# Kernel optimization log

Hardware: AMD Instinct MI355X
Metric: run time of the kernel (lower is better)

Reference implementation:

```python
import jax, jax.numpy as jnp
import numpy as np

B, P, ENC = 64, 196, 2048
ATT, DEC, EMB = 512, 512, 512
V, MAXLEN = 10000, 30


def setup_inputs() -> dict:
    key = jax.random.key(0)
    ks = jax.random.split(key, 20)
    s = 0.02
    inp = {
        "encoder_out": jax.random.normal(ks[0], (B, P, ENC), jnp.float32),
        "captions": jax.random.randint(ks[1], (B, MAXLEN), 0, V).astype(jnp.int64),
        "caption_lengths": jax.random.randint(ks[2], (B,), 1, MAXLEN).astype(jnp.int64),
        # parameters (PyTorch Linear convention: y = x @ W.T + b)
        "emb_table": jax.random.uniform(ks[3], (V, EMB), jnp.float32, -0.1, 0.1),
        "W_enc_att": jax.random.normal(ks[4], (ATT, ENC), jnp.float32) * s,
        "b_enc_att": jnp.zeros((ATT,), jnp.float32),
        "W_dec_att": jax.random.normal(ks[5], (ATT, DEC), jnp.float32) * s,
        "b_dec_att": jnp.zeros((ATT,), jnp.float32),
        "w_full_att": jax.random.normal(ks[6], (1, ATT), jnp.float32) * s,
        "b_full_att": jnp.zeros((1,), jnp.float32),
        "W_ih": jax.random.normal(ks[7], (4 * DEC, EMB + ENC), jnp.float32) * s,
        "b_ih": jnp.zeros((4 * DEC,), jnp.float32),
        "W_hh": jax.random.normal(ks[8], (4 * DEC, DEC), jnp.float32) * s,
        "b_hh": jnp.zeros((4 * DEC,), jnp.float32),
        "W_init_h": jax.random.normal(ks[9], (DEC, ENC), jnp.float32) * s,
        "b_init_h": jnp.zeros((DEC,), jnp.float32),
        "W_init_c": jax.random.normal(ks[10], (DEC, ENC), jnp.float32) * s,
        "b_init_c": jnp.zeros((DEC,), jnp.float32),
        "W_fc": jax.random.uniform(ks[11], (V, DEC), jnp.float32, -0.1, 0.1),
        "b_fc": jnp.zeros((V,), jnp.float32),
    }
    return inp


def reference(encoder_out, captions, caption_lengths, emb_table,
              W_enc_att, b_enc_att, W_dec_att, b_dec_att,
              w_full_att, b_full_att, W_ih, b_ih, W_hh, b_hh,
              W_init_h, b_init_h, W_init_c, b_init_c, W_fc, b_fc):
    # init hidden state from mean-pooled encoder features
    mean_enc = encoder_out.mean(axis=1)                       # [B, ENC]
    h0 = mean_enc @ W_init_h.T + b_init_h                     # [B, DEC]
    c0 = mean_enc @ W_init_c.T + b_init_c                     # [B, DEC]

    # encoder-side attention projection is time-invariant: hoist out of the loop
    att1 = jnp.einsum('bpe,ae->bpa', encoder_out, W_enc_att) + b_enc_att  # [B, P, ATT]

    embeddings = emb_table[captions]                          # [B, T, EMB]
    T = captions.shape[1] - 1
    emb_steps = jnp.swapaxes(embeddings[:, :T, :], 0, 1)      # [T, B, EMB]

    def step(carry, emb_t):
        h, c = carry
        att2 = h @ W_dec_att.T + b_dec_att                    # [B, ATT]
        e = (jax.nn.relu(att1 + att2[:, None, :]) @ w_full_att.T + b_full_att)[..., 0]  # [B, P]
        alpha = jax.nn.softmax(e, axis=1)                     # [B, P]
        context = jnp.einsum('bp,bpe->be', alpha, encoder_out)  # [B, ENC]
        x = jnp.concatenate([emb_t, context], axis=1)         # [B, EMB+ENC]
        gates = x @ W_ih.T + b_ih + h @ W_hh.T + b_hh         # [B, 4*DEC]
        i, f, g, o = jnp.split(gates, 4, axis=1)
        c_new = jax.nn.sigmoid(f) * c + jax.nn.sigmoid(i) * jnp.tanh(g)
        h_new = jax.nn.sigmoid(o) * jnp.tanh(c_new)
        preds = h_new @ W_fc.T + b_fc                         # dropout in eval mode = identity
        return (h_new, c_new), (preds, alpha)

    _, (preds_seq, alpha_seq) = jax.lax.scan(step, (h0, c0), emb_steps)
    predictions = jnp.swapaxes(preds_seq, 0, 1)               # [B, T, V]
    alphas = jnp.swapaxes(alpha_seq, 0, 1)                    # [B, T, P]
    return predictions, alphas
```

## Files before the change

kernel.cpp:

```cpp
#include <hip/hip_runtime.h>
#include <cstddef>

constexpr int B_   = 64;
constexpr int P_   = 196;
constexpr int ENC_ = 2048;
constexpr int ATT_ = 512;
constexpr int DEC_ = 512;
constexpr int EMB_ = 512;
constexpr int V_   = 10000;
constexpr int MAXLEN_ = 30;
constexpr int T_   = 29;
constexpr int G4_  = 2048;
constexpr int KIH_ = 2560;
constexpr int XK2_ = 2560;

constexpr int NBLK = 256;
constexpr int TPB  = 1024;
constexpr int NT   = NBLK * TPB;
constexpr int NW   = NT / 64;
constexpr int FSTR = 16;
constexpr size_t ZS_ = (size_t)B_ * G4_;
constexpr int NPT = 625;

typedef __attribute__((ext_vector_type(8))) short short8;
typedef __attribute__((ext_vector_type(4))) float f32x4;
using us = unsigned short;

__device__ __forceinline__ us f2bf(float x) {
    union { float f; unsigned u; } v; v.f = x;
    unsigned r = v.u + 0x7fff + ((v.u >> 16) & 1);
    return (us)(r >> 16);
}
__device__ __forceinline__ float bf2f(us u) {
    union { unsigned u; float f; } v; v.u = ((unsigned)u) << 16;
    return v.f;
}

__device__ __forceinline__ unsigned ld4cc(const void* p) {
    unsigned r;
    asm volatile("global_load_dword %0, %1, off sc1\n\ts_waitcnt vmcnt(0)"
                 : "=v"(r) : "v"(p) : "memory");
    return r;
}
__device__ __forceinline__ void ld4cc_x8(const float* p0, const float* p1,
                                         const float* p2, const float* p3,
                                         const float* p4, const float* p5,
                                         const float* p6, const float* p7,
                                         float* o) {
    float r0, r1, r2, r3, r4, r5, r6, r7;
    asm volatile("global_load_dword %0, %8, off sc1\n\t"
                 "global_load_dword %1, %9, off sc1\n\t"
                 "global_load_dword %2, %10, off sc1\n\t"
                 "global_load_dword %3, %11, off sc1\n\t"
                 "global_load_dword %4, %12, off sc1\n\t"
                 "global_load_dword %5, %13, off sc1\n\t"
                 "global_load_dword %6, %14, off sc1\n\t"
                 "global_load_dword %7, %15, off sc1\n\t"
                 "s_waitcnt vmcnt(0)"
                 : "=&v"(r0), "=&v"(r1), "=&v"(r2), "=&v"(r3),
                   "=&v"(r4), "=&v"(r5), "=&v"(r6), "=&v"(r7)
                 : "v"(p0), "v"(p1), "v"(p2), "v"(p3),
                   "v"(p4), "v"(p5), "v"(p6), "v"(p7) : "memory");
    o[0]=r0; o[1]=r1; o[2]=r2; o[3]=r3; o[4]=r4; o[5]=r5; o[6]=r6; o[7]=r7;
}
__device__ __forceinline__ void ld16cc_x3(const void* p0, const void* p1, const void* p2,
                                          short8* a, short8* b, short8* c) {
    short8 ra, rb, rc;
    asm volatile("global_load_dwordx4 %0, %3, off sc1\n\t"
                 "global_load_dwordx4 %1, %4, off sc1\n\t"
                 "global_load_dwordx4 %2, %5, off sc1\n\t"
                 "s_waitcnt vmcnt(0)"
                 : "=&v"(ra), "=&v"(rb), "=&v"(rc)
                 : "v"(p0), "v"(p1), "v"(p2) : "memory");
    *a = ra; *b = rb; *c = rc;
}
__device__ __forceinline__ void ld16cc_x4(const void* p0, const void* p1,
                                          const void* p2, const void* p3,
                                          short8* a, short8* b, short8* c, short8* d) {
    short8 ra, rb, rc, rd;
    asm volatile("global_load_dwordx4 %0, %4, off sc1\n\t"
                 "global_load_dwordx4 %1, %5, off sc1\n\t"
                 "global_load_dwordx4 %2, %6, off sc1\n\t"
                 "global_load_dwordx4 %3, %7, off sc1\n\t"
                 "s_waitcnt vmcnt(0)"
                 : "=&v"(ra), "=&v"(rb), "=&v"(rc), "=&v"(rd)
                 : "v"(p0), "v"(p1), "v"(p2), "v"(p3) : "memory");
    *a = ra; *b = rb; *c = rc; *d = rd;
}
__device__ __forceinline__ void ldf8cc(const void* p0, const void* p1, f32x4* a, f32x4* b) {
    f32x4 ra, rb;
    asm volatile("global_load_dwordx4 %0, %2, off sc1\n\t"
                 "global_load_dwordx4 %1, %3, off sc1\n\t"
                 "s_waitcnt vmcnt(0)"
                 : "=&v"(ra), "=&v"(rb) : "v"(p0), "v"(p1) : "memory");
    *a = ra; *b = rb;
}
__device__ __forceinline__ void st4cc(void* p, unsigned v) {
    asm volatile("global_store_dword %0, %1, off sc1" :: "v"(p), "v"(v) : "memory");
}
__device__ __forceinline__ void st2cc(void* p, unsigned v) {
    asm volatile("global_store_short %0, %1, off sc1" :: "v"(p), "v"(v) : "memory");
}
__device__ __forceinline__ float wredsum(float a) {
#pragma unroll
    for (int o = 32; o > 0; o >>= 1) a += __shfl_xor(a, o);
    return a;
}

template<bool REL>
__device__ __forceinline__ void gbar_arrive(unsigned* flags, unsigned tok) {
    asm volatile("s_waitcnt vmcnt(0)" ::: "memory");
    __syncthreads();
    if (threadIdx.x == 0)
        __hip_atomic_store(&flags[blockIdx.x * FSTR], tok,
                           REL ? __ATOMIC_RELEASE : __ATOMIC_RELAXED,
                           __HIP_MEMORY_SCOPE_AGENT);
}
__device__ __forceinline__ void gbar_wait(unsigned* flags, unsigned tok) {
    if (threadIdx.x < NBLK) {
        while (__hip_atomic_load(&flags[threadIdx.x * FSTR], __ATOMIC_RELAXED,
                                 __HIP_MEMORY_SCOPE_AGENT) < tok)
            __builtin_amdgcn_s_sleep(1);
    }
    __syncthreads();
}
template<bool REL>
__device__ __forceinline__ void gbar(unsigned* flags, unsigned tok) {
    gbar_arrive<REL>(flags, tok);
    gbar_wait(flags, tok);
}

__device__ __forceinline__ void cvt8(const float* __restrict__ src, us* __restrict__ dst) {
    const float4* p = (const float4*)src;
    float4 a = p[0], b = p[1];
    union { short8 v; us u[8]; } o;
    o.u[0] = f2bf(a.x); o.u[1] = f2bf(a.y); o.u[2] = f2bf(a.z); o.u[3] = f2bf(a.w);
    o.u[4] = f2bf(b.x); o.u[5] = f2bf(b.y); o.u[6] = f2bf(b.z); o.u[7] = f2bf(b.w);
    *(short8*)dst = o.v;
}

__device__ __forceinline__ float score8(short8 v, const f32x4& lo, const f32x4& hi,
                                        const float4& w0, const float4& w1) {
    float acc = 0.f, x;
    x = bf2f((us)v[0]) + lo[0]; acc += fmaxf(x, 0.f) * w0.x;
    x = bf2f((us)v[1]) + lo[1]; acc += fmaxf(x, 0.f) * w0.y;
    x = bf2f((us)v[2]) + lo[2]; acc += fmaxf(x, 0.f) * w0.z;
    x = bf2f((us)v[3]) + lo[3]; acc += fmaxf(x, 0.f) * w0.w;
    x = bf2f((us)v[4]) + hi[0]; acc += fmaxf(x, 0.f) * w1.x;
    x = bf2f((us)v[5]) + hi[1]; acc += fmaxf(x, 0.f) * w1.y;
    x = bf2f((us)v[6]) + hi[2]; acc += fmaxf(x, 0.f) * w1.z;
    x = bf2f((us)v[7]) + hi[3]; acc += fmaxf(x, 0.f) * w1.w;
    return acc;
}

__device__ __forceinline__ void preds_task(const us* s_h, const us* __restrict__ wfcb,
                                           const float* __restrict__ b_fc,
                                           float* __restrict__ outp,
                                           int nt, int tt, int lane) {
    const int r = lane & 15, g = lane >> 4;
    f32x4 acc[4] = {{0,0,0,0},{0,0,0,0},{0,0,0,0},{0,0,0,0}};
    const us* Brow = wfcb + (size_t)(nt*16 + r)*DEC_ + g*8;
    const us* As   = s_h + r*520 + g*8;
#pragma unroll
    for (int k0 = 0; k0 < DEC_; k0 += 64) {
        short8 b0 = *(const short8*)(Brow + k0);
        short8 b1 = *(const short8*)(Brow + k0 + 32);
#pragma unroll
        for (int mt = 0; mt < 4; ++mt) {
            short8 a0 = *(const short8*)(As + mt*16*520 + k0);
            short8 a1 = *(const short8*)(As + mt*16*520 + k0 + 32);
            acc[mt] = __builtin_amdgcn_mfma_f32_16x16x32_bf16(a0, b0, acc[mt], 0, 0, 0);
            acc[mt] = __builtin_amdgcn_mfma_f32_16x16x32_bf16(a1, b1, acc[mt], 0, 0, 0);
        }
    }
    const int n = nt*16 + r;
    const float bv = b_fc[n];
#pragma unroll
    for (int mt = 0; mt < 4; ++mt)
#pragma unroll
        for (int i = 0; i < 4; ++i) {
            int b = mt*16 + g*4 + i;
            outp[(size_t)b*(T_*V_) + (size_t)tt*V_ + n] = acc[mt][i] + bv;
        }
}

__global__ __launch_bounds__(TPB) void k_persist(
    const float* __restrict__ enc, const int* __restrict__ captions,
    const float* __restrict__ emb_table,
    const float* __restrict__ W_enc_att, const float* __restrict__ b_enc_att,
    const float* __restrict__ W_dec_att, const float* __restrict__ b_dec_att,
    const float* __restrict__ w_full,
    const float* __restrict__ W_ih, const float* __restrict__ b_ih,
    const float* __restrict__ W_hh, const float* __restrict__ b_hh,
    const float* __restrict__ W_init_h, const float* __restrict__ b_init_h,
    const float* __restrict__ W_init_c, const float* __restrict__ b_init_c,
    const float* __restrict__ W_fc, const float* __restrict__ b_fc,
    us* encb, us* wencb, us* wdecb, us* wfcb, us* wcat2, us* wembW,
    us* winitb, us* xembA, us* att1b, us* hbuf, us* xcatb, us* meanbb,
    float* cst, float* att2G, float* gp, float* gpe, float* bsum,
    unsigned* flags, float* outp, float* outa)
{
    __shared__ us s_stage[64 * 520];
    __shared__ us s_wb[64 * 328];
    __shared__ us s_wd[16 * 520];
    __shared__ float s_e[P_];
    __shared__ float s_al[P_];
    __shared__ float s_red[32];

    const int tid = threadIdx.x, bid = blockIdx.x;
    const int gtid = bid * TPB + tid;
    const int wid  = gtid >> 6;
    const int w    = tid >> 6;
    const int lane = tid & 63;
    unsigned tok = 0;
    float creg = 0.f;
    us* const hb0 = hbuf;
    us* const hb1 = hbuf + (size_t)B_ * DEC_;

    for (int i = gtid; i < B_*P_*ENC_/8; i += NT) cvt8(enc + (size_t)i*8, encb + (size_t)i*8);
    for (int i = gtid; i < ATT_*ENC_/8; i += NT) cvt8(W_enc_att + (size_t)i*8, wencb + (size_t)i*8);
    for (int i = gtid; i < ATT_*DEC_/8; i += NT) cvt8(W_dec_att + (size_t)i*8, wdecb + (size_t)i*8);
    for (int i = gtid; i < V_*DEC_/8;   i += NT) cvt8(W_fc + (size_t)i*8, wfcb + (size_t)i*8);
    for (int i = gtid; i < G4_*XK2_/8;  i += NT) {
        int n = (i*8) / XK2_, k = (i*8) % XK2_;
        const float* src = (k < ENC_) ? (W_ih + (size_t)n*KIH_ + EMB_ + k)
                                      : (W_hh + (size_t)n*DEC_ + (k - ENC_));
        cvt8(src, wcat2 + (size_t)i*8);
    }
    for (int i = gtid; i < G4_*EMB_/8;  i += NT)
        cvt8(W_ih + ((size_t)((i*8) / EMB_))*KIH_ + ((i*8) % EMB_), wembW + (size_t)i*8);
    for (int i = gtid; i < 1024*ENC_/8; i += NT) {
        int n = (i*8) >> 11, k = (i*8) & (ENC_ - 1);
        const float* src = (n < 512) ? (W_init_h + (size_t)n*ENC_ + k)
                                     : (W_init_c + (size_t)(n-512)*ENC_ + k);
        cvt8(src, winitb + (size_t)i*8);
    }
    for (int i = gtid; i < T_*B_*EMB_/8; i += NT) {
        int r = i >> 6, c8 = i & 63;
        int t = r >> 6, b = r & 63;
        int cap = captions[b*MAXLEN_ + t];
        cvt8(emb_table + (size_t)cap*EMB_ + c8*8, xembA + (size_t)r*EMB_ + c8*8);
    }
    if (gtid < G4_) bsum[gtid] = b_ih[gtid] + b_hh[gtid];
    if (gtid < B_*ENC_) {
        int b = gtid >> 11, e = gtid & (ENC_ - 1);
        const float* base = enc + (size_t)b*P_*ENC_ + e;
        float s = 0.f;
        for (int p = 0; p < P_; ++p) s += base[(size_t)p*ENC_];
        meanbb[gtid] = f2bf(s * (1.f / P_));
    }
    gbar<true>(flags, ++tok);

    for (int task = wid; task < 256 + 1856; task += NW) {
        const int r = lane & 15, g = lane >> 4;
        if (task < 256) {
            const int mt = task & 3, nt = task >> 2;
            const int m0 = mt*16, n0 = nt*16;
            const us* Ar = meanbb + (size_t)(m0 + r)*ENC_ + g*8;
            const us* Br = winitb + (size_t)(n0 + r)*ENC_ + g*8;
            f32x4 acc0 = {0,0,0,0}, acc1 = {0,0,0,0};
#pragma unroll 4
            for (int k0 = 0; k0 < ENC_; k0 += 64) {
                acc0 = __builtin_amdgcn_mfma_f32_16x16x32_bf16(
                    *(const short8*)(Ar + k0), *(const short8*)(Br + k0), acc0, 0, 0, 0);
                acc1 = __builtin_amdgcn_mfma_f32_16x16x32_bf16(
                    *(const short8*)(Ar + k0 + 32), *(const short8*)(Br + k0 + 32), acc1, 0, 0, 0);
            }
            const int n = n0 + r;
            if (n < 512) {
                float bv = b_init_h[n];
#pragma unroll
                for (int i = 0; i < 4; ++i) {
                    int b = m0 + g*4 + i;
                    unsigned hv = f2bf(acc0[i] + acc1[i] + bv);
                    st2cc(hb1 + b*DEC_ + n, hv);
                    st2cc(xcatb + (size_t)b*XK2_ + ENC_ + n, hv);
                }
            } else {
                int d = n - 512;
                float bv = b_init_c[d];
#pragma unroll
                for (int i = 0; i < 4; ++i)
                    st4cc(cst + (m0 + g*4 + i)*DEC_ + d,
                          __float_as_uint(acc0[i] + acc1[i] + bv));
            }
        } else {
            const int q = task - 256;
            const int m0 = (q >> 6) * 64, n0 = (q & 63) * 32;
            f32x4 acc[4][2] = {};
            const us* Ab = xembA + (size_t)(m0 + r)*EMB_ + g*8;
            const us* Bb = wembW + (size_t)(n0 + r)*EMB_ + g*8;
#pragma unroll 2
            for (int k0 = 0; k0 < EMB_; k0 += 32) {
                short8 af[4], bfr[2];
#pragma unroll
                for (int mi = 0; mi < 4; ++mi)
                    af[mi] = *(const short8*)(Ab + (size_t)mi*16*EMB_ + k0);
#pragma unroll
                for (int nj = 0; nj < 2; ++nj)
                    bfr[nj] = *(const short8*)(Bb + (size_t)nj*16*EMB_ + k0);
#pragma unroll
                for (int mi = 0; mi < 4; ++mi)
#pragma unroll
                    for (int nj = 0; nj < 2; ++nj)
                        acc[mi][nj] = __builtin_amdgcn_mfma_f32_16x16x32_bf16(
                            af[mi], bfr[nj], acc[mi][nj], 0, 0, 0);
            }
#pragma unroll
            for (int mi = 0; mi < 4; ++mi)
#pragma unroll
                for (int nj = 0; nj < 2; ++nj) {
                    int n = n0 + nj*16 + r;
                    float bv = bsum[n];
#pragma unroll
                    for (int i = 0; i < 4; ++i) {
                        int m = m0 + mi*16 + g*4 + i;
                        gpe[(size_t)m*G4_ + n] = acc[mi][nj][i] + bv;
                    }
                }
        }
    }
    gbar<true>(flags, ++tok);

    for (int task = wid; task < 3264; task += NW) {
        const int r = lane & 15, g = lane >> 4;
        if (task < 3136) {
            int mt = task >> 4, nt2 = task & 15;
            int m0 = mt*64, n0 = nt2*32;
            f32x4 acc[4][2] = {};
            const us* Ab = encb + (size_t)(m0 + r)*ENC_ + g*8;
            const us* Bb = wencb + (size_t)(n0 + r)*ENC_ + g*8;
#pragma unroll 2
            for (int k0 = 0; k0 < ENC_; k0 += 32) {
                short8 af[4], bfr[2];
#pragma unroll
                for (int mi = 0; mi < 4; ++mi)
                    af[mi] = *(const short8*)(Ab + (size_t)mi*16*ENC_ + k0);
#pragma unroll
                for (int nj = 0; nj < 2; ++nj)
                    bfr[nj] = *(const short8*)(Bb + (size_t)nj*16*ENC_ + k0);
#pragma unroll
                for (int mi = 0; mi < 4; ++mi)
#pragma unroll
                    for (int nj = 0; nj < 2; ++nj)
                        acc[mi][nj] = __builtin_amdgcn_mfma_f32_16x16x32_bf16(
                            af[mi], bfr[nj], acc[mi][nj], 0, 0, 0);
            }
#pragma unroll
            for (int mi = 0; mi < 4; ++mi)
#pragma unroll
                for (int nj = 0; nj < 2; ++nj) {
                    int n = n0 + nj*16 + r;
                    float bv = b_enc_att[n];
#pragma unroll
                    for (int i = 0; i < 4; ++i) {
                        int m = m0 + mi*16 + g*4 + i;
                        att1b[(size_t)m*ATT_ + n] = f2bf(acc[mi][nj][i] + bv);
                    }
                }
        } else {
            int q = task - 3136;
            int nt = q >> 2, mt = q & 3;
            const us* Ar = hb1 + (size_t)(mt*16 + r)*DEC_ + g*8;
            const us* Br = wdecb + (size_t)(nt*16 + r)*DEC_ + g*8;
            f32x4 acc0 = {0,0,0,0}, acc1 = {0,0,0,0};
#pragma unroll 4
            for (int k0 = 0; k0 < DEC_; k0 += 64) {
                short8 a0, a1, dum;
                ld16cc_x3(Ar + k0, Ar + k0 + 32, Ar + k0, &a0, &a1, &dum);
                acc0 = __builtin_amdgcn_mfma_f32_16x16x32_bf16(
                    a0, *(const short8*)(Br + k0), acc0, 0, 0, 0);
                acc1 = __builtin_amdgcn_mfma_f32_16x16x32_bf16(
                    a1, *(const short8*)(Br + k0 + 32), acc1, 0, 0, 0);
            }
            int n = nt*16 + r;
            float bv = b_dec_att[n];
#pragma unroll
            for (int i = 0; i < 4; ++i)
                st4cc(att2G + (size_t)(mt*16 + g*4 + i)*ATT_ + n,
                      __float_as_uint(acc0[i] + acc1[i] + bv));
        }
    }
    gbar<true>(flags, ++tok);

    {
        const int z = bid >> 5, nb = bid & 31;
        for (int c = tid; c < 2560; c += TPB) {
            int row = c / 40, col8 = c % 40;
            *(short8*)(s_wb + row*328 + col8*8) =
                *(const short8*)(wcat2 + (size_t)(nb*64 + row)*XK2_ + (size_t)z*320 + col8*8);
        }
        if (bid < 32)
            for (int c = tid; c < 1024; c += TPB) {
                int row = c >> 6, col8 = c & 63;
                *(short8*)(s_wd + row*520 + col8*8) =
                    *(const short8*)(wdecb + (size_t)(bid*16 + row)*DEC_ + col8*8);
            }
        if (tid < 128) creg = __uint_as_float(ld4cc(cst + bid*128 + tid));
        __syncthreads();
    }

    for (int t = 0; t < T_; ++t) {
        {
            const int b = bid & 63, cc = bid >> 6;
            f32x4 a2lo, a2hi;
            const float* ap = att2G + (size_t)b*ATT_ + lane*8;
            ldf8cc(ap, ap + 4, &a2lo, &a2hi);
            const float4 w0 = *(const float4*)(w_full + lane*8);
            const float4 w1 = *(const float4*)(w_full + lane*8 + 4);
            const us* a1base = att1b + (size_t)b*P_*ATT_ + lane*8;
            for (int p = w; p < P_; p += 32) {
                const int p2 = p + 16;
                short8 v0 = *(const short8*)(a1base + (size_t)p*ATT_);
                short8 v1 = (p2 < P_) ? *(const short8*)(a1base + (size_t)p2*ATT_) : v0;
                float acc0 = score8(v0, a2lo, a2hi, w0, w1);
                float acc1 = score8(v1, a2lo, a2hi, w0, w1);
                acc0 = wredsum(acc0);
                acc1 = wredsum(acc1);
                if (lane == 0) {
                    s_e[p] = acc0;
                    if (p2 < P_) s_e[p2] = acc1;
                }
            }
            __syncthreads();
            float v = (tid < P_) ? s_e[tid] : -3.4e38f;
            float mx = v;
#pragma unroll
            for (int o = 32; o > 0; o >>= 1) mx = fmaxf(mx, __shfl_xor(mx, o));
            if (lane == 0) s_red[w] = mx;
            __syncthreads();
            mx = s_red[0];
#pragma unroll
            for (int j = 1; j < 16; ++j) mx = fmaxf(mx, s_red[j]);
            float ev = (tid < P_) ? expf(v - mx) : 0.f;
            float sm = wredsum(ev);
            if (lane == 0) s_red[16 + w] = sm;
            __syncthreads();
            float tot = 0.f;
#pragma unroll
            for (int j = 0; j < 16; ++j) tot += s_red[16 + j];
            if (tid < P_) {
                float al = ev / tot;
                s_al[tid] = al;
                if (cc == 0) outa[((size_t)b*T_ + t)*P_ + tid] = al;
            }
            __syncthreads();
            float a[8] = {};
            const us* ep = encb + (size_t)b*P_*ENC_ + cc*512 + lane*8;
            for (int p = w; p < P_; p += 16) {
                short8 vv = *(const short8*)(ep + (size_t)p*ENC_);
                float al = s_al[p];
#pragma unroll
                for (int j = 0; j < 8; ++j) a[j] += al * bf2f((us)vv[j]);
            }
            float* s_accf = (float*)s_stage;
            {
                f32x4 lo = {a[0],a[1],a[2],a[3]}, hi = {a[4],a[5],a[6],a[7]};
                *(f32x4*)(s_accf + w*512 + lane*8)     = lo;
                *(f32x4*)(s_accf + w*512 + lane*8 + 4) = hi;
            }
            __syncthreads();
            if (tid < 256) {
                int c2 = tid*2;
                float s0 = 0.f, s1 = 0.f;
#pragma unroll
                for (int q = 0; q < 16; ++q) {
                    s0 += s_accf[q*512 + c2];
                    s1 += s_accf[q*512 + c2 + 1];
                }
                unsigned pk = (unsigned)f2bf(s0) | ((unsigned)f2bf(s1) << 16);
                st4cc(xcatb + (size_t)b*XK2_ + cc*512 + c2, pk);
            }
            __syncthreads();
        }
        gbar<false>(flags, ++tok);

        {
            const int z = bid >> 5;
            {
                short8 v0, v1, v2;
                int c0 = tid, c1 = tid + 1024, c2i = tid + 2048;
                const us* p0 = xcatb + (size_t)(c0/40)*XK2_ + z*320 + (c0%40)*8;
                const us* p1 = xcatb + (size_t)(c1/40)*XK2_ + z*320 + (c1%40)*8;
                bool has2 = c2i < 2560;
                const us* p2 = has2 ? xcatb + (size_t)(c2i/40)*XK2_ + z*320 + (c2i%40)*8 : p0;
                ld16cc_x3(p0, p1, p2, &v0, &v1, &v2);
                *(short8*)(s_stage + (c0/40)*328 + (c0%40)*8) = v0;
                *(short8*)(s_stage + (c1/40)*328 + (c1%40)*8) = v1;
                if (has2) *(short8*)(s_stage + (c2i/40)*328 + (c2i%40)*8) = v2;
            }
            __syncthreads();
            const int nt = (bid & 31)*4 + (w >> 2), mt = w & 3;
            const int r = lane & 15, g = lane >> 4;
            const us* sxr = s_stage + (mt*16 + r)*328 + g*8;
            const us* Br  = s_wb + ((w >> 2)*16 + r)*328 + g*8;
            f32x4 acc0 = {0,0,0,0}, acc1 = {0,0,0,0};
#pragma unroll
            for (int k0 = 0; k0 < 320; k0 += 64) {
                acc0 = __builtin_amdgcn_mfma_f32_16x16x32_bf16(
                    *(const short8*)(sxr + k0), *(const short8*)(Br + k0), acc0, 0, 0, 0);
                acc1 = __builtin_amdgcn_mfma_f32_16x16x32_bf16(
                    *(const short8*)(sxr + k0 + 32), *(const short8*)(Br + k0 + 32), acc1, 0, 0, 0);
            }
            const int n = nt*16 + r;
#pragma unroll
            for (int i = 0; i < 4; ++i) {
                int m = mt*16 + g*4 + i;
                st4cc(gp + ZS_*z + (size_t)m*G4_ + n, __float_as_uint(acc0[i] + acc1[i]));
            }
            __syncthreads();
        }
        gbar<false>(flags, ++tok);

        {
            float* sg = (float*)s_stage;
            if (tid < 512) {
                const int cell = tid & 127, gate = tid >> 7;
                const int idx = bid*128 + cell;
                const int b = idx >> 9, d = idx & 511;
                const float* gz = gp + (size_t)b*G4_ + gate*512 + d;
                float vz[8];
                ld4cc_x8(gz, gz + ZS_, gz + 2*ZS_, gz + 3*ZS_,
                         gz + 4*ZS_, gz + 5*ZS_, gz + 6*ZS_, gz + 7*ZS_, vz);
                sg[tid] = ((vz[0]+vz[1]) + (vz[2]+vz[3])) + ((vz[4]+vz[5]) + (vz[6]+vz[7]));
            }
            __syncthreads();
            if (tid < 128) {
                const int idx = bid*128 + tid;
                const int b = idx >> 9, d = idx & 511;
                const float* ge = gpe + ((size_t)(t*B_ + b))*G4_ + d;
                float gi = sg[tid]       + ge[0];
                float gf = sg[128 + tid] + ge[512];
                float gg = sg[256 + tid] + ge[1024];
                float go = sg[384 + tid] + ge[1536];
                float si = 1.f / (1.f + expf(-gi));
                float sf = 1.f / (1.f + expf(-gf));
                float so = 1.f / (1.f + expf(-go));
                float cn = sf * creg + si * tanhf(gg);
                creg = cn;
                float hn = so * tanhf(cn);
                unsigned hv = f2bf(hn);
                us* hnew = (t & 1) ? hb1 : hb0;
                st2cc(hnew + idx, hv);
                st2cc(xcatb + (size_t)b*XK2_ + ENC_ + d, hv);
            }
        }
        gbar<false>(flags, ++tok);

        if (t != T_ - 1) {
            ++tok;
            if (bid < 32) {
                {
                    const us* hbn = (t & 1) ? hb1 : hb0;
                    short8 v0, v1, v2, v3;
                    int c0 = tid, c1 = tid + 1024, c2i = tid + 2048, c3 = tid + 3072;
                    ld16cc_x4(hbn + (c0>>6)*DEC_ + (c0&63)*8, hbn + (c1>>6)*DEC_ + (c1&63)*8,
                              hbn + (c2i>>6)*DEC_ + (c2i&63)*8, hbn + (c3>>6)*DEC_ + (c3&63)*8,
                              &v0, &v1, &v2, &v3);
                    *(short8*)(s_stage + (c0>>6)*520 + (c0&63)*8) = v0;
                    *(short8*)(s_stage + (c1>>6)*520 + (c1&63)*8) = v1;
                    *(short8*)(s_stage + (c2i>>6)*520 + (c2i&63)*8) = v2;
                    *(short8*)(s_stage + (c3>>6)*520 + (c3&63)*8) = v3;
                }
                __syncthreads();
                if (w < 4) {
                    const int r = lane & 15, g = lane >> 4;
                    const us* As = s_stage + (w*16 + r)*520 + g*8;
                    const us* Bs = s_wd + r*520 + g*8;
                    f32x4 acc0 = {0,0,0,0}, acc1 = {0,0,0,0};
#pragma unroll
                    for (int k0 = 0; k0 < DEC_; k0 += 64) {
                        acc0 = __builtin_amdgcn_mfma_f32_16x16x32_bf16(
                            *(const short8*)(As + k0), *(const short8*)(Bs + k0), acc0, 0, 0, 0);
                        acc1 = __builtin_amdgcn_mfma_f32_16x16x32_bf16(
                            *(const short8*)(As + k0 + 32), *(const short8*)(Bs + k0 + 32), acc1, 0, 0, 0);
                    }
                    const int n = bid*16 + r;
                    float bv = b_dec_att[n];
#pragma unroll
                    for (int i = 0; i < 4; ++i)
                        st4cc(att2G + (size_t)(w*16 + g*4 + i)*ATT_ + n,
                              __float_as_uint(acc0[i] + acc1[i] + bv));
                }
                gbar_arrive<false>(flags, tok);
                gbar_wait(flags, tok);
            } else {
                gbar_arrive<false>(flags, tok);
                if (t > 0) {
                    const us* hbo = (t & 1) ? hb0 : hb1;
                    short8 v0, v1, v2, v3;
                    int c0 = tid, c1 = tid + 1024, c2i = tid + 2048, c3 = tid + 3072;
                    ld16cc_x4(hbo + (c0>>6)*DEC_ + (c0&63)*8, hbo + (c1>>6)*DEC_ + (c1&63)*8,
                              hbo + (c2i>>6)*DEC_ + (c2i&63)*8, hbo + (c3>>6)*DEC_ + (c3&63)*8,
                              &v0, &v1, &v2, &v3);
                    *(short8*)(s_stage + (c0>>6)*520 + (c0&63)*8) = v0;
                    *(short8*)(s_stage + (c1>>6)*520 + (c1&63)*8) = v1;
                    *(short8*)(s_stage + (c2i>>6)*520 + (c2i&63)*8) = v2;
                    *(short8*)(s_stage + (c3>>6)*520 + (c3&63)*8) = v3;
                    __syncthreads();
                    const int tq = (bid - 32)*3 + w;
                    if (w < 3 && tq < NPT)
                        preds_task(s_stage, wfcb, b_fc, outp, tq, t - 1, lane);
                }
                gbar_wait(flags, tok);
            }
        } else {
            if (bid >= 32) {
                const us* hbo = (t & 1) ? hb0 : hb1;
                short8 v0, v1, v2, v3;
                int c0 = tid, c1 = tid + 1024, c2i = tid + 2048, c3 = tid + 3072;
                ld16cc_x4(hbo + (c0>>6)*DEC_ + (c0&63)*8, hbo + (c1>>6)*DEC_ + (c1&63)*8,
                          hbo + (c2i>>6)*DEC_ + (c2i&63)*8, hbo + (c3>>6)*DEC_ + (c3&63)*8,
                          &v0, &v1, &v2, &v3);
                *(short8*)(s_stage + (c0>>6)*520 + (c0&63)*8) = v0;
                *(short8*)(s_stage + (c1>>6)*520 + (c1&63)*8) = v1;
                *(short8*)(s_stage + (c2i>>6)*520 + (c2i&63)*8) = v2;
                *(short8*)(s_stage + (c3>>6)*520 + (c3&63)*8) = v3;
                __syncthreads();
                const int tq = (bid - 32)*3 + w;
                if (w < 3 && tq < NPT)
                    preds_task(s_stage, wfcb, b_fc, outp, tq, t - 1, lane);
            }
        }
    }

    if (bid < 40) {
        __syncthreads();
        const us* hbn = ((T_ - 1) & 1) ? hb1 : hb0;
        {
            short8 v0, v1, v2, v3;
            int c0 = tid, c1 = tid + 1024, c2i = tid + 2048, c3 = tid + 3072;
            ld16cc_x4(hbn + (c0>>6)*DEC_ + (c0&63)*8, hbn + (c1>>6)*DEC_ + (c1&63)*8,
                      hbn + (c2i>>6)*DEC_ + (c2i&63)*8, hbn + (c3>>6)*DEC_ + (c3&63)*8,
                      &v0, &v1, &v2, &v3);
            *(short8*)(s_stage + (c0>>6)*520 + (c0&63)*8) = v0;
            *(short8*)(s_stage + (c1>>6)*520 + (c1&63)*8) = v1;
            *(short8*)(s_stage + (c2i>>6)*520 + (c2i&63)*8) = v2;
            *(short8*)(s_stage + (c3>>6)*520 + (c3&63)*8) = v3;
        }
        __syncthreads();
        const int tq = bid*16 + w;
        if (tq < NPT)
            preds_task(s_stage, wfcb, b_fc, outp, tq, T_ - 1, lane);
    }
}

extern "C" void kernel_launch(void* const* d_in, const int* in_sizes, int n_in,
                              void* d_out, int out_size, void* d_ws, size_t ws_size,
                              hipStream_t stream) {
    const float* enc       = (const float*)d_in[0];
    const int*   captions  = (const int*)d_in[1];
    const float* emb_table = (const float*)d_in[3];
    const float* W_enc_att = (const float*)d_in[4];
    const float* b_enc_att = (const float*)d_in[5];
    const float* W_dec_att = (const float*)d_in[6];
    const float* b_dec_att = (const float*)d_in[7];
    const float* w_full    = (const float*)d_in[8];
    const float* W_ih      = (const float*)d_in[10];
    const float* b_ih      = (const float*)d_in[11];
    const float* W_hh      = (const float*)d_in[12];
    const float* b_hh      = (const float*)d_in[13];
    const float* W_init_h  = (const float*)d_in[14];
    const float* b_init_h  = (const float*)d_in[15];
    const float* W_init_c  = (const float*)d_in[16];
    const float* b_init_c  = (const float*)d_in[17];
    const float* W_fc      = (const float*)d_in[18];
    const float* b_fc      = (const float*)d_in[19];

    char* ws = (char*)d_ws;
    size_t off = 0;
    auto alloc = [&](size_t bytes) {
        void* p = ws + off;
        off = (off + bytes + 255) & ~(size_t)255;
        return p;
    };
    us* encb   = (us*)alloc((size_t)B_ * P_ * ENC_ * 2);
    us* wencb  = (us*)alloc((size_t)ATT_ * ENC_ * 2);
    us* wdecb  = (us*)alloc((size_t)ATT_ * DEC_ * 2);
    us* wfcb   = (us*)alloc((size_t)V_ * DEC_ * 2);
    us* wcat2  = (us*)alloc((size_t)G4_ * XK2_ * 2);
    us* wembW  = (us*)alloc((size_t)G4_ * EMB_ * 2);
    us* winitb = (us*)alloc((size_t)1024 * ENC_ * 2);
    us* xembA  = (us*)alloc((size_t)T_ * B_ * EMB_ * 2);
    us* att1b  = (us*)alloc((size_t)B_ * P_ * ATT_ * 2);
    us* hbuf   = (us*)alloc((size_t)2 * B_ * DEC_ * 2);
    us* xcatb  = (us*)alloc((size_t)B_ * XK2_ * 2);
    us* meanbb = (us*)alloc((size_t)B_ * ENC_ * 2);
    float* cst   = (float*)alloc((size_t)B_ * DEC_ * 4);
    float* att2G = (float*)alloc((size_t)B_ * ATT_ * 4);
    float* gp    = (float*)alloc((size_t)B_ * G4_ * 8 * 4);
    float* gpe   = (float*)alloc((size_t)T_ * B_ * G4_ * 4);
    float* bsum  = (float*)alloc((size_t)G4_ * 4);
    unsigned* flags = (unsigned*)alloc((size_t)(NBLK + 1) * FSTR * 4);

    float* outp = (float*)d_out;
    float* outa = outp + (size_t)B_ * T_ * V_;

    hipMemsetAsync(flags, 0, (NBLK + 1) * FSTR * sizeof(unsigned), stream);
    k_persist<<<NBLK, TPB, 0, stream>>>(
        enc, captions, emb_table, W_enc_att, b_enc_att, W_dec_att, b_dec_att,
        w_full, W_ih, b_ih, W_hh, b_hh, W_init_h, b_init_h, W_init_c, b_init_c,
        W_fc, b_fc,
        encb, wencb, wdecb, wfcb, wcat2, wembW, winitb, xembA, att1b, hbuf, xcatb,
        meanbb, cst, att2G, gp, gpe, bsum, flags, outp, outa);
}
```

Before: 1.204 ms.

## Fuse att2 projection into LSTM cell blocks as split-K partials, drop a grid barrier

Each block that produces a slice of the new hidden state now computes a partial att2 product (a 128-wide K chunk of W_dec_att) right away and writes it to a partial-sum buffer. The attention stage later sums the four partials when it loads att2. This removes the separate att2 MFMA phase on 32 blocks and one grid-wide barrier per timestep, and spreads the fc prediction work across all blocks. The trade-off is scalar FMA work reading W_dec_att from global memory in every block, four times the att2 loads, and some added per-block latency before the barrier.

```diff
diff --git a/kernel.cpp b/kernel.cpp
--- a/kernel.cpp
+++ b/kernel.cpp
@@ -87,13 +87,24 @@
                  : "v"(p0), "v"(p1), "v"(p2), "v"(p3) : "memory");
     *a = ra; *b = rb; *c = rc; *d = rd;
 }
-__device__ __forceinline__ void ldf8cc(const void* p0, const void* p1, f32x4* a, f32x4* b) {
-    f32x4 ra, rb;
-    asm volatile("global_load_dwordx4 %0, %2, off sc1\n\t"
-                 "global_load_dwordx4 %1, %3, off sc1\n\t"
+__device__ __forceinline__ void ld_att2sum(const float* ap, f32x4* lo, f32x4* hi) {
+    f32x4 a0, b0, a1, b1, a2, b2, a3, b3;
+    asm volatile("global_load_dwordx4 %0, %8, off sc1\n\t"
+                 "global_load_dwordx4 %1, %9, off sc1\n\t"
+                 "global_load_dwordx4 %2, %10, off sc1\n\t"
+                 "global_load_dwordx4 %3, %11, off sc1\n\t"
+                 "global_load_dwordx4 %4, %12, off sc1\n\t"
+                 "global_load_dwordx4 %5, %13, off sc1\n\t"
+                 "global_load_dwordx4 %6, %14, off sc1\n\t"
+                 "global_load_dwordx4 %7, %15, off sc1\n\t"
                  "s_waitcnt vmcnt(0)"
-                 : "=&v"(ra), "=&v"(rb) : "v"(p0), "v"(p1) : "memory");
-    *a = ra; *b = rb;
+                 : "=&v"(a0), "=&v"(b0), "=&v"(a1), "=&v"(b1),
+                   "=&v"(a2), "=&v"(b2), "=&v"(a3), "=&v"(b3)
+                 : "v"(ap), "v"(ap + 4), "v"(ap + 512), "v"(ap + 516),
+                   "v"(ap + 1024), "v"(ap + 1028), "v"(ap + 1536), "v"(ap + 1540)
+                 : "memory");
+    *lo = (a0 + a1) + (a2 + a3);
+    *hi = (b0 + b1) + (b2 + b3);
 }
 __device__ __forceinline__ void st4cc(void* p, unsigned v) {
     asm volatile("global_store_dword %0, %1, off sc1" :: "v"(p), "v"(v) : "memory");
@@ -197,12 +208,12 @@
     const float* __restrict__ W_fc, const float* __restrict__ b_fc,
     us* encb, us* wencb, us* wdecb, us* wfcb, us* wcat2, us* wembW,
     us* winitb, us* xembA, us* att1b, us* hbuf, us* xcatb, us* meanbb,
-    float* cst, float* att2G, float* gp, float* gpe, float* bsum,
+    float* cst, float* att2P, float* gp, float* gpe, float* bsum,
     unsigned* flags, float* outp, float* outa)
 {
     __shared__ us s_stage[64 * 520];
     __shared__ us s_wb[64 * 328];
-    __shared__ us s_wd[16 * 520];
+    __shared__ float s_hq[128];
     __shared__ float s_e[P_];
     __shared__ float s_al[P_];
     __shared__ float s_red[32];
@@ -242,6 +253,7 @@
         cvt8(emb_table + (size_t)cap*EMB_ + c8*8, xembA + (size_t)r*EMB_ + c8*8);
     }
     if (gtid < G4_) bsum[gtid] = b_ih[gtid] + b_hh[gtid];
+    if (gtid < B_*4*ATT_) att2P[gtid] = 0.f;
     if (gtid < B_*ENC_) {
         int b = gtid >> 11, e = gtid & (ENC_ - 1);
         const float* base = enc + (size_t)b*P_*ENC_ + e;
@@ -377,7 +389,7 @@
             float bv = b_dec_att[n];
 #pragma unroll
             for (int i = 0; i < 4; ++i)
-                st4cc(att2G + (size_t)(mt*16 + g*4 + i)*ATT_ + n,
+                st4cc(att2P + (size_t)(mt*16 + g*4 + i)*(4*ATT_) + n,
                       __float_as_uint(acc0[i] + acc1[i] + bv));
         }
     }
@@ -390,12 +402,6 @@
             *(short8*)(s_wb + row*328 + col8*8) =
                 *(const short8*)(wcat2 + (size_t)(nb*64 + row)*XK2_ + (size_t)z*320 + col8*8);
         }
-        if (bid < 32)
-            for (int c = tid; c < 1024; c += TPB) {
-                int row = c >> 6, col8 = c & 63;
-                *(short8*)(s_wd + row*520 + col8*8) =
-                    *(const short8*)(wdecb + (size_t)(bid*16 + row)*DEC_ + col8*8);
-            }
         if (tid < 128) creg = __uint_as_float(ld4cc(cst + bid*128 + tid));
         __syncthreads();
     }
@@ -404,8 +410,7 @@
         {
             const int b = bid & 63, cc = bid >> 6;
             f32x4 a2lo, a2hi;
-            const float* ap = att2G + (size_t)b*ATT_ + lane*8;
-            ldf8cc(ap, ap + 4, &a2lo, &a2hi);
+            ld_att2sum(att2P + (size_t)b*(4*ATT_) + lane*8, &a2lo, &a2hi);
             const float4 w0 = *(const float4*)(w_full + lane*8);
             const float4 w1 = *(const float4*)(w_full + lane*8 + 4);
             const us* a1base = att1b + (size_t)b*P_*ATT_ + lane*8;
@@ -543,69 +548,27 @@
                 us* hnew = (t & 1) ? hb1 : hb0;
                 st2cc(hnew + idx, hv);
                 st2cc(xcatb + (size_t)b*XK2_ + ENC_ + d, hv);
-            }
-        }
-        gbar<false>(flags, ++tok);
-
-        if (t != T_ - 1) {
+                s_hq[tid] = bf2f((us)hv);
+            }
+            __syncthreads();
+            if (tid < 512) {
+                const int q = bid & 3;
+                const us* wr = wdecb + (size_t)tid*DEC_ + q*128;
+                float acc = (q == 0) ? b_dec_att[tid] : 0.f;
+#pragma unroll
+                for (int j = 0; j < 16; ++j) {
+                    short8 wv = *(const short8*)(wr + j*8);
+#pragma unroll
+                    for (int e = 0; e < 8; ++e)
+                        acc += s_hq[j*8 + e] * bf2f((us)wv[e]);
+                }
+                st4cc(att2P + (size_t)bid*512 + tid, __float_as_uint(acc));
+            }
+        }
+        {
             ++tok;
-            if (bid < 32) {
-                {
-                    const us* hbn = (t & 1) ? hb1 : hb0;
-                    short8 v0, v1, v2, v3;
-                    int c0 = tid, c1 = tid + 1024, c2i = tid + 2048, c3 = tid + 3072;
-                    ld16cc_x4(hbn + (c0>>6)*DEC_ + (c0&63)*8, hbn + (c1>>6)*DEC_ + (c1&63)*8,
-                              hbn + (c2i>>6)*DEC_ + (c2i&63)*8, hbn + (c3>>6)*DEC_ + (c3&63)*8,
-                              &v0, &v1, &v2, &v3);
-                    *(short8*)(s_stage + (c0>>6)*520 + (c0&63)*8) = v0;
-                    *(short8*)(s_stage + (c1>>6)*520 + (c1&63)*8) = v1;
-                    *(short8*)(s_stage + (c2i>>6)*520 + (c2i&63)*8) = v2;
-                    *(short8*)(s_stage + (c3>>6)*520 + (c3&63)*8) = v3;
-                }
-                __syncthreads();
-                if (w < 4) {
-                    const int r = lane & 15, g = lane >> 4;
-                    const us* As = s_stage + (w*16 + r)*520 + g*8;
-                    const us* Bs = s_wd + r*520 + g*8;
-                    f32x4 acc0 = {0,0,0,0}, acc1 = {0,0,0,0};
-#pragma unroll
-                    for (int k0 = 0; k0 < DEC_; k0 += 64) {
-                        acc0 = __builtin_amdgcn_mfma_f32_16x16x32_bf16(
-                            *(const short8*)(As + k0), *(const short8*)(Bs + k0), acc0, 0, 0, 0);
-                        acc1 = __builtin_amdgcn_mfma_f32_16x16x32_bf16(
-                            *(const short8*)(As + k0 + 32), *(const short8*)(Bs + k0 + 32), acc1, 0, 0, 0);
-                    }
-                    const int n = bid*16 + r;
-                    float bv = b_dec_att[n];
-#pragma unroll
-                    for (int i = 0; i < 4; ++i)
-                        st4cc(att2G + (size_t)(w*16 + g*4 + i)*ATT_ + n,
-                              __float_as_uint(acc0[i] + acc1[i] + bv));
-                }
-                gbar_arrive<false>(flags, tok);
-                gbar_wait(flags, tok);
-            } else {
-                gbar_arrive<false>(flags, tok);
-                if (t > 0) {
-                    const us* hbo = (t & 1) ? hb0 : hb1;
-                    short8 v0, v1, v2, v3;
-                    int c0 = tid, c1 = tid + 1024, c2i = tid + 2048, c3 = tid + 3072;
-                    ld16cc_x4(hbo + (c0>>6)*DEC_ + (c0&63)*8, hbo + (c1>>6)*DEC_ + (c1&63)*8,
-                              hbo + (c2i>>6)*DEC_ + (c2i&63)*8, hbo + (c3>>6)*DEC_ + (c3&63)*8,
-                              &v0, &v1, &v2, &v3);
-                    *(short8*)(s_stage + (c0>>6)*520 + (c0&63)*8) = v0;
-                    *(short8*)(s_stage + (c1>>6)*520 + (c1&63)*8) = v1;
-                    *(short8*)(s_stage + (c2i>>6)*520 + (c2i&63)*8) = v2;
-                    *(short8*)(s_stage + (c3>>6)*520 + (c3&63)*8) = v3;
-                    __syncthreads();
-                    const int tq = (bid - 32)*3 + w;
-                    if (w < 3 && tq < NPT)
-                        preds_task(s_stage, wfcb, b_fc, outp, tq, t - 1, lane);
-                }
-                gbar_wait(flags, tok);
-            }
-        } else {
-            if (bid >= 32) {
+            gbar_arrive<false>(flags, tok);
+            if (t > 0) {
                 const us* hbo = (t & 1) ? hb0 : hb1;
                 short8 v0, v1, v2, v3;
                 int c0 = tid, c1 = tid + 1024, c2i = tid + 2048, c3 = tid + 3072;
@@ -617,30 +580,28 @@
                 *(short8*)(s_stage + (c2i>>6)*520 + (c2i&63)*8) = v2;
                 *(short8*)(s_stage + (c3>>6)*520 + (c3&63)*8) = v3;
                 __syncthreads();
-                const int tq = (bid - 32)*3 + w;
+                const int tq = bid*3 + w;
                 if (w < 3 && tq < NPT)
                     preds_task(s_stage, wfcb, b_fc, outp, tq, t - 1, lane);
             }
-        }
-    }
-
-    if (bid < 40) {
+            gbar_wait(flags, tok);
+        }
+    }
+
+    {
+        const us* hbn = ((T_ - 1) & 1) ? hb1 : hb0;
+        short8 v0, v1, v2, v3;
+        int c0 = tid, c1 = tid + 1024, c2i = tid + 2048, c3 = tid + 3072;
+        ld16cc_x4(hbn + (c0>>6)*DEC_ + (c0&63)*8, hbn + (c1>>6)*DEC_ + (c1&63)*8,
+                  hbn + (c2i>>6)*DEC_ + (c2i&63)*8, hbn + (c3>>6)*DEC_ + (c3&63)*8,
+                  &v0, &v1, &v2, &v3);
+        *(short8*)(s_stage + (c0>>6)*520 + (c0&63)*8) = v0;
+        *(short8*)(s_stage + (c1>>6)*520 + (c1&63)*8) = v1;
+        *(short8*)(s_stage + (c2i>>6)*520 + (c2i&63)*8) = v2;
+        *(short8*)(s_stage + (c3>>6)*520 + (c3&63)*8) = v3;
         __syncthreads();
-        const us* hbn = ((T_ - 1) & 1) ? hb1 : hb0;
-        {
-            short8 v0, v1, v2, v3;
-            int c0 = tid, c1 = tid + 1024, c2i = tid + 2048, c3 = tid + 3072;
-            ld16cc_x4(hbn + (c0>>6)*DEC_ + (c0&63)*8, hbn + (c1>>6)*DEC_ + (c1&63)*8,
-                      hbn + (c2i>>6)*DEC_ + (c2i&63)*8, hbn + (c3>>6)*DEC_ + (c3&63)*8,
-                      &v0, &v1, &v2, &v3);
-            *(short8*)(s_stage + (c0>>6)*520 + (c0&63)*8) = v0;
-            *(short8*)(s_stage + (c1>>6)*520 + (c1&63)*8) = v1;
-            *(short8*)(s_stage + (c2i>>6)*520 + (c2i&63)*8) = v2;
-            *(short8*)(s_stage + (c3>>6)*520 + (c3&63)*8) = v3;
-        }
-        __syncthreads();
-        const int tq = bid*16 + w;
-        if (tq < NPT)
+        const int tq = bid*3 + w;
+        if (w < 3 && tq < NPT)
             preds_task(s_stage, wfcb, b_fc, outp, tq, T_ - 1, lane);
     }
 }
@@ -687,7 +648,7 @@
     us* xcatb  = (us*)alloc((size_t)B_ * XK2_ * 2);
     us* meanbb = (us*)alloc((size_t)B_ * ENC_ * 2);
     float* cst   = (float*)alloc((size_t)B_ * DEC_ * 4);
-    float* att2G = (float*)alloc((size_t)B_ * ATT_ * 4);
+    float* att2P = (float*)alloc((size_t)B_ * 4 * ATT_ * 4);
     float* gp    = (float*)alloc((size_t)B_ * G4_ * 8 * 4);
     float* gpe   = (float*)alloc((size_t)T_ * B_ * G4_ * 4);
     float* bsum  = (float*)alloc((size_t)G4_ * 4);
@@ -702,5 +663,5 @@
         w_full, W_ih, b_ih, W_hh, b_hh, W_init_h, b_init_h, W_init_c, b_init_c,
         W_fc, b_fc,
         encb, wencb, wdecb, wfcb, wcat2, wembW, winitb, xembA, att1b, hbuf, xcatb,
-        meanbb, cst, att2G, gp, gpe, bsum, flags, outp, outa);
-}
+        meanbb, cst, att2P, gp, gpe, bsum, flags, outp, outa);
+}
```

New measurement: 1.439 ms. +19.5%, slower.
